# Kernel tuning notes

Hardware: AMD Instinct MI355X
Metric: run time of the kernel (lower is better)

## Reference

```python
import jax, jax.numpy as jnp
import numpy as np


def ctc_neg_log_likelihood(log_probs, labels, input_lengths, label_lengths, blank=0):
    """Per-sample CTC negative log likelihood (torch.nn.CTCLoss semantics,
    zero_infinity=True). log_probs: (T, B, V) log-softmax; labels: (B, L) int."""
    T, B, V = log_probs.shape
    L = labels.shape[1]
    S = 2 * L + 1  # extended label sequence with interleaved blanks
    NEG = jnp.asarray(-1e9, log_probs.dtype)
    # extended labels: blank at even positions, label at odd positions -> (B, S)
    ext = jnp.full((B, S), blank, dtype=labels.dtype).at[:, 1::2].set(labels)
    # log prob of each extended symbol at each time: (T, B, S)
    lp_ext = jnp.take_along_axis(log_probs, jnp.broadcast_to(ext[None].astype(jnp.int32), (T, B, S)), axis=2)
    # skip transition s-2 -> s allowed iff ext[s] != blank and ext[s] != ext[s-2]
    skip = jnp.concatenate(
        [jnp.zeros((B, 2), bool), (ext[:, 2:] != blank) & (ext[:, 2:] != ext[:, :-2])], axis=1)
    alpha0 = jnp.full((B, S), NEG).at[:, 0].set(lp_ext[0, :, 0]).at[:, 1].set(lp_ext[0, :, 1])

    def step(alpha, inp):
        lp_t, t = inp
        s1 = jnp.concatenate([jnp.full((B, 1), NEG), alpha[:, :-1]], axis=1)
        s2 = jnp.where(skip, jnp.concatenate([jnp.full((B, 2), NEG), alpha[:, :-2]], axis=1), NEG)
        new = jnp.logaddexp(jnp.logaddexp(alpha, s1), s2) + lp_t
        # frames beyond each sample's input length leave alpha unchanged
        alpha = jnp.where((t < input_lengths)[:, None], new, alpha)
        return alpha, None

    alpha, _ = jax.lax.scan(step, alpha0, (lp_ext[1:], jnp.arange(1, T)))
    i1 = (2 * label_lengths.astype(jnp.int32) - 1)[:, None]
    a_last = jnp.take_along_axis(alpha, i1, axis=1)[:, 0]
    a_blank = jnp.take_along_axis(alpha, i1 + 1, axis=1)[:, 0]
    nll = -jnp.logaddexp(a_last, a_blank)
    # zero_infinity=True: infeasible alignments contribute 0
    return jnp.where(nll > 1e8, jnp.zeros_like(nll), nll)


def setup_inputs() -> dict:
    B, T, D, V, L = 32, 2048, 512, 5, 256
    key = jax.random.key(0)
    k1, k2, k3, k4, k5 = jax.random.split(key, 5)
    hs_pad = jax.random.normal(k1, (B, T, D), dtype=jnp.float32)
    W = jax.random.normal(k2, (D, V), dtype=jnp.float32) * 0.02
    b = jnp.zeros((V,), dtype=jnp.float32)
    hlens = jax.random.randint(k3, (B,), 1024, T + 1, dtype=jnp.int32)
    ys_pad = jax.random.randint(k4, (B, L), 1, V, dtype=jnp.int32)  # labels never equal blank=0
    ys_lens = jax.random.randint(k5, (B,), 64, L + 1, dtype=jnp.int32)
    return {"hs_pad": hs_pad, "W": W, "b": b, "hlens": hlens, "ys_pad": ys_pad, "ys_lens": ys_lens}


def reference(hs_pad, W, b, hlens, ys_pad, ys_lens):
    B = hs_pad.shape[0]
    logits = jnp.einsum('btd,dv->btv', hs_pad, W) + b      # ctc_lo (dropout p=0)
    logits_tbv = jnp.transpose(logits, (1, 0, 2))          # (T, B, V)
    log_probs = jax.nn.log_softmax(logits_tbv, axis=2)
    probs = jnp.exp(log_probs)                             # == softmax(logits)
    per_sample = ctc_neg_log_likelihood(log_probs, ys_pad, hlens, ys_lens, blank=0)
    loss = jnp.sum(per_sample) / B                         # sum-reduced CTC / batch size
    ys_hat = jnp.transpose(log_probs, (1, 0, 2))           # (B, T, V)
    no_log_ys_hat = jnp.transpose(probs, (1, 0, 2))        # (B, T, V)
    return loss, ys_hat, no_log_ys_hat
```

## Files before the change

### kernel.cpp

```cpp
#include <hip/hip_runtime.h>
#include <math.h>

#define B_DIM 32
#define T_DIM 2048
#define D_DIM 512
#define V_DIM 5
#define L_DIM 256
#define LN2D 0.6931471805599453
#define TP (T_DIM + 4)

typedef const float __attribute__((address_space(1)))* gas_fp;
typedef float __attribute__((address_space(3)))* las_fp;

__device__ __forceinline__ float dpp_shr1_f32(float x) {
    return __int_as_float(__builtin_amdgcn_update_dpp(
        0, __float_as_int(x), 0x138, 0xf, 0xf, true));
}
__device__ __forceinline__ int dpp_shr1_i32(int x) {
    return __builtin_amdgcn_update_dpp(0, x, 0x138, 0xf, 0xf, true);
}
__device__ __forceinline__ float wave_fsum_dpp(float x) {
    x += __int_as_float(__builtin_amdgcn_update_dpp(0, __float_as_int(x), 0x111, 0xf, 0xf, true));
    x += __int_as_float(__builtin_amdgcn_update_dpp(0, __float_as_int(x), 0x112, 0xf, 0xf, true));
    x += __int_as_float(__builtin_amdgcn_update_dpp(0, __float_as_int(x), 0x114, 0xf, 0xf, true));
    x += __int_as_float(__builtin_amdgcn_update_dpp(0, __float_as_int(x), 0x118, 0xf, 0xf, true));
    x += __int_as_float(__builtin_amdgcn_update_dpp(0, __float_as_int(x), 0x142, 0xa, 0xf, false));
    x += __int_as_float(__builtin_amdgcn_update_dpp(0, __float_as_int(x), 0x143, 0xc, 0xf, false));
    return x;
}

__global__ __launch_bounds__(256) void k_logits_softmax(
    const float* __restrict__ hs, const float* __restrict__ W,
    const float* __restrict__ bias, float* __restrict__ logp,
    float* __restrict__ probs)
{
    const int lane = threadIdx.x & 63;
    const int wid  = (blockIdx.x * blockDim.x + threadIdx.x) >> 6;
    const int nwav = (gridDim.x * blockDim.x) >> 6;

    float wr[2][4][V_DIM];
#pragma unroll
    for (int c = 0; c < 2; ++c)
#pragma unroll
        for (int j = 0; j < 4; ++j) {
            const int k = c * 256 + lane * 4 + j;
#pragma unroll
            for (int v = 0; v < V_DIM; ++v) wr[c][j][v] = W[k * V_DIM + v];
        }
    float br[V_DIM];
#pragma unroll
    for (int v = 0; v < V_DIM; ++v) br[v] = bias[v];

    for (int row = wid; row < B_DIM * T_DIM; row += nwav) {
        const float* x = hs + (size_t)row * D_DIM;
        float4 xa = *reinterpret_cast<const float4*>(x + lane * 4);
        float4 xb = *reinterpret_cast<const float4*>(x + 256 + lane * 4);
        const float xs0[4] = {xa.x, xa.y, xa.z, xa.w};
        const float xs1[4] = {xb.x, xb.y, xb.z, xb.w};

        float acc[V_DIM];
#pragma unroll
        for (int v = 0; v < V_DIM; ++v) acc[v] = 0.f;
#pragma unroll
        for (int j = 0; j < 4; ++j)
#pragma unroll
            for (int v = 0; v < V_DIM; ++v) {
                acc[v] = fmaf(xs0[j], wr[0][j][v], acc[v]);
                acc[v] = fmaf(xs1[j], wr[1][j][v], acc[v]);
            }
#pragma unroll
        for (int v = 0; v < V_DIM; ++v) acc[v] = wave_fsum_dpp(acc[v]);

        if (lane == 63) {
#pragma unroll
            for (int v = 0; v < V_DIM; ++v) acc[v] += br[v];
            float m = fmaxf(fmaxf(fmaxf(acc[0], acc[1]), fmaxf(acc[2], acc[3])), acc[4]);
            float e[V_DIM], s = 0.f;
#pragma unroll
            for (int v = 0; v < V_DIM; ++v) { e[v] = __expf(acc[v] - m); s += e[v]; }
            float lse = m + __logf(s);
            float inv = 1.f / s;
            size_t base = (size_t)row * V_DIM;
#pragma unroll
            for (int v = 0; v < V_DIM; ++v) {
                logp[base + v]  = acc[v] - lse;
                probs[base + v] = e[v] * inv;
            }
        }
    }
}

__global__ __launch_bounds__(64) void k_ctc(
    const float* __restrict__ probs, const int* __restrict__ ys_pad,
    const int* __restrict__ hlens, const int* __restrict__ ys_lens,
    float* __restrict__ nll_out)
{
    __shared__ float  s_probs[T_DIM * V_DIM];
    __shared__ __align__(16) float s_pT[4][TP];
    __shared__ float  s_beta[513];
    __shared__ int    s_E[64];
    __shared__ double s_red[64];

    const int b    = blockIdx.x;
    const int lane = threadIdx.x;
    const int hlen = hlens[b];
    const int lb   = ys_lens[b];
    const int Sb   = 2 * lb + 1;
    const float* pb = probs + (size_t)b * T_DIM * V_DIM;
    const int*  yrow = ys_pad + b * L_DIM;

    for (int i = 0; i < (T_DIM * V_DIM) / 64; ++i) {
        __builtin_amdgcn_global_load_lds((gas_fp)(pb + i * 64 + lane),
                                         (las_fp)(&s_probs[i * 64]), 4, 0, 0);
    }
    asm volatile("s_waitcnt vmcnt(0)" ::: "memory");

    double lg2 = 0.0;
    for (int i = 0; i < T_DIM / 64; ++i) {
        const int t = i * 64 + lane;
        const float* sp = &s_probs[t * 5];
        const float p0 = sp[0];
        const float inv = 1.0f / p0;
        s_pT[0][t + 3] = sp[1] * inv;
        s_pT[1][t + 3] = sp[2] * inv;
        s_pT[2][t + 3] = sp[3] * inv;
        s_pT[3][t + 3] = sp[4] * inv;
        if (t < hlen) {
            int ee; float mm = frexpf(p0, &ee);
            lg2 += (double)ee + (double)__log2f(mm);
        }
    }

    const int y0 = yrow[4 * lane + 0];
    const int y1 = yrow[4 * lane + 1];
    const int y2 = yrow[4 * lane + 2];
    const int y3 = yrow[4 * lane + 3];
    const int ym1 = (lane > 0) ? yrow[4 * lane - 1] : -1;

    const float sk0 = ((lane > 0) && (y0 != ym1)) ? 1.f : 0.f;
    const float sk1 = (y1 != y0) ? 1.f : 0.f;
    const float sk2 = (y2 != y1) ? 1.f : 0.f;
    const float sk3 = (y3 != y2) ? 1.f : 0.f;

    bool vmask[9];
#pragma unroll
    for (int i = 0; i < 9; ++i) vmask[i] = (8 * lane + i) < Sb;

    float aA[9], aB[9];
#pragma unroll
    for (int i = 0; i < 9; ++i) aA[i] = 0.f;
    if (lane == 0) {
        aA[0] = 1.f;
        aA[1] = s_pT[y0 - 1][3];
    }
    int E = 0;
    int delta = 0;

    const float* q_y0 = &s_pT[y0 - 1][0];
    const float* q_y1 = &s_pT[y1 - 1][0];
    const float* q_y2 = &s_pT[y2 - 1][0];
    const float* q_y3 = &s_pT[y3 - 1][0];

#define LD4F(d, p)                                                        \
    { float4 u_ = *(const float4*)(p);                                    \
      (d)[0] = u_.x; (d)[1] = u_.y; (d)[2] = u_.z; (d)[3] = u_.w; }

#define LOADQ(dst, kk)                                                    \
    { const int off_ = 4 + 4 * (kk);                                      \
      LD4F(dst + 0,  q_y0 + off_); LD4F(dst + 4,  q_y1 + off_);           \
      LD4F(dst + 8,  q_y2 + off_); LD4F(dst + 12, q_y3 + off_); }

#define STEPX(O, N, L, s_)                                                \
    {                                                                     \
        float p7_ = ldexpf(dpp_shr1_f32(O[7]), delta);                    \
        N[7] = fmaf(sk3, O[5], O[7] + O[6]) * L[12 + (s_)];               \
        N[2] = O[2] + O[1];                                               \
        N[3] = fmaf(sk1, O[1], O[3] + O[2]) * L[4 + (s_)];                \
        N[4] = O[4] + O[3];                                               \
        N[5] = fmaf(sk2, O[3], O[5] + O[4]) * L[8 + (s_)];                \
        N[6] = O[6] + O[5];                                               \
        N[8] = O[8] + O[7];                                               \
        N[0] = O[0] + p7_;                                                \
        N[1] = fmaf(sk0, p7_, O[1] + O[0]) * L[0 + (s_)];                 \
    }

#define STEP4(L)                                                          \
    STEPX(aA, aB, L, 0); STEPX(aB, aA, L, 1);                             \
    STEPX(aA, aB, L, 2); STEPX(aB, aA, L, 3);

#define RENORM()                                                          \
    {                                                                     \
        float m_ = 0.f;                                                   \
        _Pragma("unroll")                                                 \
        for (int i_ = 0; i_ < 9; ++i_)                                    \
            m_ = vmask[i_] ? fmaxf(m_, aA[i_]) : m_;                      \
        const bool big_ = (m_ >= 1e-12f);                                 \
        int em_ = (__float_as_int(m_) >> 23) & 0xff;                      \
        em_ = em_ > 253 ? 253 : em_;                                      \
        const float sc_ = __int_as_float((254 - (big_ ? em_ : 127)) << 23); \
        _Pragma("unroll")                                                 \
        for (int i_ = 0; i_ < 9; ++i_)                                    \
            aA[i_] = big_ ? aA[i_] * sc_ : 0.f;                           \
        const int En_ = E + (big_ ? em_ - 127 : 0);                       \
        const int up_ = dpp_shr1_i32(En_);                                \
        E = (!big_ && lane > 0) ? (up_ - 32) : En_;                       \
        const int upE_ = dpp_shr1_i32(E);                                 \
        int d_ = upE_ - E;                                                \
        d_ = d_ > 52 ? 52 : d_;                                           \
        d_ = d_ < -126 ? -126 : d_;                                       \
        delta = d_;                                                       \
    }

    const int NS = hlen - 1;
    const int nfull = NS >> 2;
    float lpA[16], lpB[16];
    LOADQ(lpA, 0);

    int blk = 0;
    for (; blk + 2 <= nfull; blk += 2) {
        LOADQ(lpB, blk + 1);
        STEP4(lpA);
        LOADQ(lpA, blk + 2);
        STEP4(lpB);
        RENORM();
    }
    if (blk < nfull) {
        STEP4(lpA);
    }
    for (int tt = 4 * nfull + 1; tt <= NS; ++tt) {
        float lt[16];
        lt[0]  = s_pT[y0 - 1][tt + 3];
        lt[4]  = s_pT[y1 - 1][tt + 3];
        lt[8]  = s_pT[y2 - 1][tt + 3];
        lt[12] = s_pT[y3 - 1][tt + 3];
        STEPX(aA, aB, lt, 0);
#pragma unroll
        for (int i = 0; i < 9; ++i) aA[i] = aB[i];
    }

#pragma unroll
    for (int i = 0; i < 8; ++i) s_beta[8 * lane + i] = aA[i];
    if (lane == 63) s_beta[512] = aA[8];
    s_E[lane] = E;
    s_red[lane] = lg2;
    __syncthreads();
    if (lane == 0) {
        double lg2tot = 0.0;
        for (int i = 0; i < 64; ++i) lg2tot += s_red[i];
        const int i1 = 2 * lb - 1, i2 = 2 * lb;
        int l1 = i1 >> 3; if (l1 > 63) l1 = 63;
        int l2 = i2 >> 3; if (l2 > 63) l2 = 63;
        const int E1 = s_E[l1], E2 = s_E[l2];
        const int Em = (E1 > E2) ? E1 : E2;
        double s = ldexp((double)s_beta[i1], E1 - Em)
                 + ldexp((double)s_beta[i2], E2 - Em);
        double nlld = -(log(s) + ((double)Em + lg2tot) * LN2D);
        float nll = (float)nlld;
        if (!(fabsf(nll) < 1e8f)) nll = 0.f;
        nll_out[b] = nll;
    }
#undef STEPX
#undef STEP4
#undef LOADQ
#undef LD4F
#undef RENORM
}

__global__ __launch_bounds__(64) void k_finalize(
    const float* __restrict__ nll, float* __restrict__ out)
{
    int tid = threadIdx.x;
    float v = (tid < B_DIM) ? nll[tid] : 0.f;
#pragma unroll
    for (int off = 32; off; off >>= 1) v += __shfl_down(v, off, 64);
    if (tid == 0) out[0] = v / (float)B_DIM;
}

extern "C" void kernel_launch(void* const* d_in, const int* in_sizes, int n_in,
                              void* d_out, int out_size, void* d_ws, size_t ws_size,
                              hipStream_t stream) {
    const float* hs      = (const float*)d_in[0];
    const float* W       = (const float*)d_in[1];
    const float* bias    = (const float*)d_in[2];
    const int*   hlens   = (const int*)d_in[3];
    const int*   ys_pad  = (const int*)d_in[4];
    const int*   ys_lens = (const int*)d_in[5];

    float* out   = (float*)d_out;
    float* logp  = out + 1;
    float* probs = out + 1 + (size_t)B_DIM * T_DIM * V_DIM;
    float* nll   = (float*)d_ws;

    hipLaunchKernelGGL(k_logits_softmax, dim3(1024), dim3(256), 0, stream,
                       hs, W, bias, logp, probs);
    hipLaunchKernelGGL(k_ctc, dim3(B_DIM), dim3(64), 0, stream,
                       probs, ys_pad, hlens, ys_lens, nll);
    hipLaunchKernelGGL(k_finalize, dim3(1), dim3(64), 0, stream, nll, out);
}
```

Before: 143.6 us.

## Mask invalid CTC states via zero row, multiply-scale carry, 8-step groups

Lanes whose states lie beyond the valid extended length now read emission probabilities from a zeroed row, so the masked max and the masked zeroing in renormalisation can be dropped. The per-step ldexpf on the neighbour carry becomes a multiply by a precomputed power-of-two scale folded into an fma. The recurrence processes 8 timesteps per loaded group with renormalisation every 8 steps, and the underflow offset is adjusted to match. This removes instructions from the serial alpha recursion at the cost of more registers for the larger prefetch buffers.

```diff
diff --git a/kernel.cpp b/kernel.cpp
--- a/kernel.cpp
+++ b/kernel.cpp
@@ -96,7 +96,7 @@
     float* __restrict__ nll_out)
 {
     __shared__ float  s_probs[T_DIM * V_DIM];
-    __shared__ __align__(16) float s_pT[4][TP];
+    __shared__ __align__(16) float s_pT[5][TP];
     __shared__ float  s_beta[513];
     __shared__ int    s_E[64];
     __shared__ double s_red[64];
@@ -114,6 +114,8 @@
                                          (las_fp)(&s_probs[i * 64]), 4, 0, 0);
     }
     asm volatile("s_waitcnt vmcnt(0)" ::: "memory");
+
+    for (int i = lane; i < TP; i += 64) s_pT[4][i] = 0.f;
 
     double lg2 = 0.0;
     for (int i = 0; i < T_DIM / 64; ++i) {
@@ -142,9 +144,10 @@
     const float sk2 = (y2 != y1) ? 1.f : 0.f;
     const float sk3 = (y3 != y2) ? 1.f : 0.f;
 
-    bool vmask[9];
-#pragma unroll
-    for (int i = 0; i < 9; ++i) vmask[i] = (8 * lane + i) < Sb;
+    const float* q_y0 = (8 * lane + 1 < Sb) ? &s_pT[y0 - 1][0] : &s_pT[4][0];
+    const float* q_y1 = (8 * lane + 3 < Sb) ? &s_pT[y1 - 1][0] : &s_pT[4][0];
+    const float* q_y2 = (8 * lane + 5 < Sb) ? &s_pT[y2 - 1][0] : &s_pT[4][0];
+    const float* q_y3 = (8 * lane + 7 < Sb) ? &s_pT[y3 - 1][0] : &s_pT[4][0];
 
     float aA[9], aB[9];
 #pragma unroll
@@ -154,25 +157,23 @@
         aA[1] = s_pT[y0 - 1][3];
     }
     int E = 0;
-    int delta = 0;
-
-    const float* q_y0 = &s_pT[y0 - 1][0];
-    const float* q_y1 = &s_pT[y1 - 1][0];
-    const float* q_y2 = &s_pT[y2 - 1][0];
-    const float* q_y3 = &s_pT[y3 - 1][0];
+    float ds = 1.f;
+    float skd0 = sk0;
 
 #define LD4F(d, p)                                                        \
     { float4 u_ = *(const float4*)(p);                                    \
       (d)[0] = u_.x; (d)[1] = u_.y; (d)[2] = u_.z; (d)[3] = u_.w; }
 
-#define LOADQ(dst, kk)                                                    \
-    { const int off_ = 4 + 4 * (kk);                                      \
-      LD4F(dst + 0,  q_y0 + off_); LD4F(dst + 4,  q_y1 + off_);           \
-      LD4F(dst + 8,  q_y2 + off_); LD4F(dst + 12, q_y3 + off_); }
+#define LOADO(dst, gg)                                                    \
+    { const int off_ = 4 + 8 * (gg);                                      \
+      LD4F(dst + 0,  q_y0 + off_); LD4F(dst + 16, q_y0 + off_ + 4);       \
+      LD4F(dst + 4,  q_y1 + off_); LD4F(dst + 20, q_y1 + off_ + 4);       \
+      LD4F(dst + 8,  q_y2 + off_); LD4F(dst + 24, q_y2 + off_ + 4);       \
+      LD4F(dst + 12, q_y3 + off_); LD4F(dst + 28, q_y3 + off_ + 4); }
 
 #define STEPX(O, N, L, s_)                                                \
     {                                                                     \
-        float p7_ = ldexpf(dpp_shr1_f32(O[7]), delta);                    \
+        float p7_ = dpp_shr1_f32(O[7]);                                   \
         N[7] = fmaf(sk3, O[5], O[7] + O[6]) * L[12 + (s_)];               \
         N[2] = O[2] + O[1];                                               \
         N[3] = fmaf(sk1, O[1], O[3] + O[2]) * L[4 + (s_)];                \
@@ -180,59 +181,62 @@
         N[5] = fmaf(sk2, O[3], O[5] + O[4]) * L[8 + (s_)];                \
         N[6] = O[6] + O[5];                                               \
         N[8] = O[8] + O[7];                                               \
-        N[0] = O[0] + p7_;                                                \
-        N[1] = fmaf(sk0, p7_, O[1] + O[0]) * L[0 + (s_)];                 \
-    }
-
-#define STEP4(L)                                                          \
-    STEPX(aA, aB, L, 0); STEPX(aB, aA, L, 1);                             \
-    STEPX(aA, aB, L, 2); STEPX(aB, aA, L, 3);
+        N[0] = fmaf(p7_, ds, O[0]);                                       \
+        N[1] = fmaf(skd0, p7_, O[1] + O[0]) * L[0 + (s_)];                \
+    }
+
+#define STEP8(L)                                                          \
+    STEPX(aA, aB, L, 0);  STEPX(aB, aA, L, 1);                            \
+    STEPX(aA, aB, L, 2);  STEPX(aB, aA, L, 3);                            \
+    STEPX(aA, aB, L, 16); STEPX(aB, aA, L, 17);                           \
+    STEPX(aA, aB, L, 18); STEPX(aB, aA, L, 19);
 
 #define RENORM()                                                          \
     {                                                                     \
-        float m_ = 0.f;                                                   \
+        float m_ = aA[0];                                                 \
         _Pragma("unroll")                                                 \
-        for (int i_ = 0; i_ < 9; ++i_)                                    \
-            m_ = vmask[i_] ? fmaxf(m_, aA[i_]) : m_;                      \
+        for (int i_ = 1; i_ < 9; ++i_) m_ = fmaxf(m_, aA[i_]);            \
         const bool big_ = (m_ >= 1e-12f);                                 \
         int em_ = (__float_as_int(m_) >> 23) & 0xff;                      \
         em_ = em_ > 253 ? 253 : em_;                                      \
         const float sc_ = __int_as_float((254 - (big_ ? em_ : 127)) << 23); \
         _Pragma("unroll")                                                 \
-        for (int i_ = 0; i_ < 9; ++i_)                                    \
-            aA[i_] = big_ ? aA[i_] * sc_ : 0.f;                           \
+        for (int i_ = 0; i_ < 9; ++i_) aA[i_] *= sc_;                     \
         const int En_ = E + (big_ ? em_ - 127 : 0);                       \
         const int up_ = dpp_shr1_i32(En_);                                \
-        E = (!big_ && lane > 0) ? (up_ - 32) : En_;                       \
+        E = (!big_ && lane > 0) ? (up_ - 16) : En_;                       \
         const int upE_ = dpp_shr1_i32(E);                                 \
         int d_ = upE_ - E;                                                \
         d_ = d_ > 52 ? 52 : d_;                                           \
         d_ = d_ < -126 ? -126 : d_;                                       \
-        delta = d_;                                                       \
+        ds = __int_as_float((127 + d_) << 23);                            \
+        skd0 = sk0 * ds;                                                  \
     }
 
     const int NS = hlen - 1;
-    const int nfull = NS >> 2;
-    float lpA[16], lpB[16];
-    LOADQ(lpA, 0);
-
-    int blk = 0;
-    for (; blk + 2 <= nfull; blk += 2) {
-        LOADQ(lpB, blk + 1);
-        STEP4(lpA);
-        LOADQ(lpA, blk + 2);
-        STEP4(lpB);
+    const int ngrp = NS >> 3;
+    float lpA[32], lpB[32];
+    LOADO(lpA, 0);
+
+    int g = 0;
+    for (; g + 2 <= ngrp; g += 2) {
+        LOADO(lpB, g + 1);
+        STEP8(lpA);
         RENORM();
-    }
-    if (blk < nfull) {
-        STEP4(lpA);
-    }
-    for (int tt = 4 * nfull + 1; tt <= NS; ++tt) {
+        LOADO(lpA, g + 2);
+        STEP8(lpB);
+        RENORM();
+    }
+    if (g < ngrp) {
+        STEP8(lpA);
+        RENORM();
+    }
+    for (int tt = 8 * ngrp + 1; tt <= NS; ++tt) {
         float lt[16];
-        lt[0]  = s_pT[y0 - 1][tt + 3];
-        lt[4]  = s_pT[y1 - 1][tt + 3];
-        lt[8]  = s_pT[y2 - 1][tt + 3];
-        lt[12] = s_pT[y3 - 1][tt + 3];
+        lt[0]  = q_y0[tt + 3];
+        lt[4]  = q_y1[tt + 3];
+        lt[8]  = q_y2[tt + 3];
+        lt[12] = q_y3[tt + 3];
         STEPX(aA, aB, lt, 0);
 #pragma unroll
         for (int i = 0; i < 9; ++i) aA[i] = aB[i];
@@ -260,8 +264,8 @@
         nll_out[b] = nll;
     }
 #undef STEPX
-#undef STEP4
-#undef LOADQ
+#undef STEP8
+#undef LOADO
 #undef LD4F
 #undef RENORM
 }
```

After: 127.4 us, median of 2. 11.3% less time.
